# Kernel tuning notes

Measured on AMD Instinct MI355X. Metric: run time of the kernel, lower is better.

The kernel has to match this reference:

```python
import jax, jax.numpy as jnp
import numpy as np

B, S, D = 2, 2048, 1024
H = 16
HD = D // H

def setup_inputs() -> dict:
    key = jax.random.key(0)
    ks = jax.random.split(key, 9)
    s = 1.0 / np.sqrt(D)
    return {
        "x": jax.random.normal(ks[0], (B, S, D), dtype=jnp.float32),
        "Wq": jax.random.normal(ks[1], (D, D), dtype=jnp.float32) * s,
        "bq": jnp.zeros((D,), dtype=jnp.float32),
        "Wk": jax.random.normal(ks[2], (D, D), dtype=jnp.float32) * s,
        "bk": jnp.zeros((D,), dtype=jnp.float32),
        "Wv": jax.random.normal(ks[3], (D, D), dtype=jnp.float32) * s,
        "bv": jnp.zeros((D,), dtype=jnp.float32),
        "Wo": jax.random.normal(ks[4], (D, D), dtype=jnp.float32) * s,
        "bo": jnp.zeros((D,), dtype=jnp.float32),
    }

def reference(x, Wq, bq, Wk, bk, Wv, bv, Wo, bo):
    b, s, d = x.shape
    # torch Linear: y = x @ W.T + b
    def proj(W, bias):
        y = jnp.einsum('bsd,ed->bse', x, W) + bias
        return y.reshape(b, s, H, HD).transpose(0, 2, 1, 3)  # [b,h,s,hd]
    Q = proj(Wq, bq)
    K = proj(Wk, bk)
    V = proj(Wv, bv)
    scale = 1.0 / jnp.sqrt(jnp.float32(HD))
    scores = jnp.einsum('bhqd,bhkd->bhqk', Q, K) * scale  # [b,h,s,s]
    attn = jax.nn.softmax(scores, axis=-1)
    out = jnp.einsum('bhqk,bhkd->bhqd', attn, V)  # [b,h,s,hd]
    out = out.transpose(0, 2, 1, 3).reshape(b, s, d)
    return jnp.einsum('bsd,ed->bse', out, Wo) + bo
```

## Files before the change

kernel.cpp:

```cpp
#include <hip/hip_runtime.h>
#include <stdint.h>


typedef __bf16 bf16x8 __attribute__((ext_vector_type(8)));
typedef float  f32x4  __attribute__((ext_vector_type(4)));
typedef unsigned short u16x8 __attribute__((ext_vector_type(8)));

#define LOG2E 1.44269504088896f
#define FIXED_MAX_BITS 14.4269504088896f

__device__ __forceinline__ unsigned short f2bf(float f) {
    union { float f; unsigned u; } v; v.f = f;
    unsigned r = v.u + 0x7FFFu + ((v.u >> 16) & 1u);
    return (unsigned short)(r >> 16);
}
__device__ __forceinline__ float bf2f(unsigned short u) {
    union { unsigned u; float f; } v; v.u = (unsigned)u << 16; return v.f;
}

__device__ __forceinline__ float exp2_fast(float x) {
#if __has_builtin(__builtin_amdgcn_exp2f)
    return __builtin_amdgcn_exp2f(x);
#else
    return __expf(x * 0.69314718056f);
#endif
}

__device__ __forceinline__ void glds16(const void* g, void* l) {
    __builtin_amdgcn_global_load_lds(
        (__attribute__((address_space(1))) void*)(g),
        (__attribute__((address_space(3))) void*)(l),
        16, 0, 0);
}

__global__ __launch_bounds__(256) void cvt_all(
    const float* __restrict__ x,  const float* __restrict__ Wq,
    const float* __restrict__ Wk, const float* __restrict__ Wv,
    const float* __restrict__ Wo,
    unsigned short* __restrict__ xb,  unsigned short* __restrict__ Wqb,
    unsigned short* __restrict__ Wkb, unsigned short* __restrict__ Wvb,
    unsigned short* __restrict__ Wob)
{
    const int stride = gridDim.x * blockDim.x;
    for (int i = blockIdx.x * blockDim.x + threadIdx.x; i < 2097152; i += stride) {
        const float* src; unsigned short* dst; int j;
        if (i < 1048576) { src = x; dst = xb; j = i; }
        else {
            int t = (i - 1048576) >> 18; j = (i - 1048576) & 262143;
            src = (t == 0) ? Wq : (t == 1) ? Wk : (t == 2) ? Wv : Wo;
            dst = (t == 0) ? Wqb : (t == 1) ? Wkb : (t == 2) ? Wvb : Wob;
        }
        float4 v = ((const float4*)src)[j];
        ushort4 o;
        o.x = f2bf(v.x); o.y = f2bf(v.y); o.z = f2bf(v.z); o.w = f2bf(v.w);
        ((ushort4*)dst)[j] = o;
    }
}

template <int MODE>
__global__ __launch_bounds__(256) void gemm_bt(
    const unsigned short* __restrict__ A,
    const unsigned short* __restrict__ W0,
    const unsigned short* __restrict__ W1,
    const unsigned short* __restrict__ W2,
    const float* __restrict__ b0,
    const float* __restrict__ b1,
    const float* __restrict__ b2,
    unsigned short* __restrict__ outQ,
    unsigned short* __restrict__ outK,
    unsigned short* __restrict__ outV,
    float* __restrict__ outF)
{
    constexpr int BM = (MODE == 0) ? 128 : 64;
    constexpr int FM = BM / 32;
    constexpr int RA = BM / 32;

    __shared__ __attribute__((aligned(16))) unsigned short As[BM * 64];
    __shared__ __attribute__((aligned(16))) unsigned short Bs[128 * 64];

    const int tid  = threadIdx.x;
    const int lane = tid & 63;
    const int wid  = tid >> 6;
    const int quad = lane >> 4;
    const int l16  = lane & 15;

    const int m0 = blockIdx.x * BM;

    const unsigned short* W;
    const float* bias;
    int proj, n0;
    if (MODE == 0) {
        proj = blockIdx.y >> 3;
        n0   = (blockIdx.y & 7) * 128;
        W    = (proj == 0) ? W0 : (proj == 1) ? W1 : W2;
        bias = (proj == 0) ? b0 : (proj == 1) ? b1 : b2;
    } else {
        proj = 0;
        n0   = blockIdx.y * 128;
        W    = W0;
        bias = b0;
    }

    const int wm = (wid >> 1) * (BM / 2);
    const int wn = (wid & 1) * 64;

    f32x4 acc[FM][4];
#pragma unroll
    for (int i = 0; i < FM; ++i)
#pragma unroll
        for (int j = 0; j < 4; ++j)
            acc[i][j] = (f32x4){0.f, 0.f, 0.f, 0.f};

    char* AsB  = (char*)As;
    char* BsB  = (char*)Bs;
    char* ldsA = AsB + wid * 1024;
    char* ldsB = BsB + wid * 1024;

    for (int k0 = 0; k0 < 1024; k0 += 64) {
#pragma unroll
        for (int q = 0; q < RA; ++q) {
            int i   = q * 256 + tid;
            int row = i >> 3;
            int sc  = (i & 7) ^ (row & 7);
            glds16(A + (size_t)(m0 + row) * 1024 + k0 + sc * 8, ldsA + q * 4096);
        }
#pragma unroll
        for (int q = 0; q < 4; ++q) {
            int i   = q * 256 + tid;
            int row = i >> 3;
            int sc  = (i & 7) ^ (row & 7);
            glds16(W + (size_t)(n0 + row) * 1024 + k0 + sc * 8, ldsB + q * 4096);
        }
        __syncthreads();

#pragma unroll
        for (int kh = 0; kh < 2; ++kh) {
            bf16x8 af[FM], bfr[4];
#pragma unroll
            for (int t = 0; t < FM; ++t) {
                int r = wm + t * 16 + l16;
                int c = (kh * 4 + quad) ^ (r & 7);
                af[t] = *(const bf16x8*)(AsB + r * 128 + c * 16);
            }
#pragma unroll
            for (int t = 0; t < 4; ++t) {
                int r = wn + t * 16 + l16;
                int c = (kh * 4 + quad) ^ (r & 7);
                bfr[t] = *(const bf16x8*)(BsB + r * 128 + c * 16);
            }
#pragma unroll
            for (int i = 0; i < FM; ++i)
#pragma unroll
                for (int j = 0; j < 4; ++j)
                    acc[i][j] = __builtin_amdgcn_mfma_f32_16x16x32_bf16(
                        af[i], bfr[j], acc[i][j], 0, 0, 0);
        }
        __syncthreads();
    }

#pragma unroll
    for (int i = 0; i < FM; ++i) {
        const int mrow0 = m0 + wm + i * 16 + quad * 4;
#pragma unroll
        for (int j = 0; j < 4; ++j) {
            const int n  = n0 + wn + j * 16 + l16;
            const float bb = bias[n];
            if (MODE == 1) {
#pragma unroll
                for (int r = 0; r < 4; ++r)
                    outF[(size_t)(mrow0 + r) * 1024 + n] = acc[i][j][r] + bb;
            } else {
                const int h = n >> 6, hd = n & 63;
                if (proj == 2) {
                    const int b = mrow0 >> 11, s = mrow0 & 2047;
                    ushort4 pk;
                    pk.x = f2bf(acc[i][j][0] + bb);
                    pk.y = f2bf(acc[i][j][1] + bb);
                    pk.z = f2bf(acc[i][j][2] + bb);
                    pk.w = f2bf(acc[i][j][3] + bb);
                    *(ushort4*)(outV + ((size_t)((b * 16 + h) * 64 + hd)) * 2048 + s) = pk;
                } else {
                    unsigned short* dst = (proj == 0) ? outQ : outK;
                    const float scl = (proj == 0) ? (0.125f * LOG2E) : 1.0f;
#pragma unroll
                    for (int r = 0; r < 4; ++r) {
                        const int m = mrow0 + r;
                        const int b = m >> 11, s = m & 2047;
                        dst[((size_t)((b * 16 + h) * 2048 + s)) * 64 + hd] =
                            f2bf((acc[i][j][r] + bb) * scl);
                    }
                }
            }
        }
    }
}

__global__ __launch_bounds__(256, 4) void attn_kernel(
    const unsigned short* __restrict__ Qb,
    const unsigned short* __restrict__ Kb,
    const unsigned short* __restrict__ Vtb,
    unsigned short* __restrict__ OP,
    float* __restrict__ LS)
{
    __shared__ __attribute__((aligned(16))) unsigned short Ks[128 * 64];
    __shared__ __attribute__((aligned(16))) unsigned short Vs[2 * 64 * 64];

    const int tid  = threadIdx.x;
    const int lane = tid & 63;
    const int wid  = tid >> 6;
    const int quad = lane >> 4;
    const int l16  = lane & 15;
    const int l7   = l16 & 7;

    const int half = blockIdx.x & 1;
    const int q0   = (blockIdx.x >> 1) * 128 + wid * 32;
    const int hb   = blockIdx.y;
    const int bq   = hb >> 4, hh = hb & 15;

    const unsigned short* Qh  = Qb  + (size_t)hb * 2048 * 64;
    const unsigned short* Kh  = Kb  + (size_t)hb * 2048 * 64;
    const unsigned short* Vth = Vtb + (size_t)hb * 64 * 2048;

    bf16x8 qf[2][2];
#pragma unroll
    for (int qt = 0; qt < 2; ++qt) {
        const unsigned short* qp = Qh + (size_t)(q0 + qt * 16 + l16) * 64 + quad * 8;
        qf[qt][0] = *(const bf16x8*)(qp);
        qf[qt][1] = *(const bf16x8*)(qp + 32);
    }

    f32x4 o[4][2];
#pragma unroll
    for (int ht = 0; ht < 4; ++ht)
#pragma unroll
        for (int qt = 0; qt < 2; ++qt)
            o[ht][qt] = (f32x4){0.f, 0.f, 0.f, 0.f};
    float lsum[2] = {0.f, 0.f};

    char* KsB  = (char*)Ks;
    char* ldsK = KsB + wid * 1024;

    const int base_row = 8 * (l16 >> 2) + (l16 & 3);
    const int kp0 = ((quad) ^ l7) * 16;
    const int kp1 = ((4 + quad) ^ l7) * 16;
    const int vrow = l16 * 128;

    const int kc0 = half * 1024;
    for (int kc = kc0; kc < kc0 + 1024; kc += 128) {
#pragma unroll
        for (int q = 0; q < 4; ++q) {
            int i   = q * 256 + tid;
            int row = i >> 3;
            int g   = (row & 3) | (((row >> 3) & 1) << 2);
            int ch  = (i & 7) ^ g;
            glds16(Kh + (size_t)(kc + row) * 64 + ch * 8, ldsK + q * 4096);
        }
#pragma unroll
        for (int sub = 0; sub < 2; ++sub)
#pragma unroll
            for (int q = 0; q < 2; ++q) {
                int i   = q * 256 + tid;
                int row = i >> 3;
                int ch  = (i & 7) ^ (row & 7);
                glds16(Vth + (size_t)row * 2048 + kc + sub * 64 + ch * 8,
                       (char*)Vs + sub * 8192 + wid * 1024 + q * 4096);
            }
        __syncthreads();

#pragma unroll
        for (int st32 = 0; st32 < 4; ++st32) {
            const char* krb = KsB + (st32 * 32 + base_row) * 128;
            bf16x8 kf00 = *(const bf16x8*)(krb + kp0);
            bf16x8 kf01 = *(const bf16x8*)(krb + kp1);
            bf16x8 kf10 = *(const bf16x8*)(krb + 512 + kp0);
            bf16x8 kf11 = *(const bf16x8*)(krb + 512 + kp1);

            const f32x4 mi = (f32x4){-FIXED_MAX_BITS, -FIXED_MAX_BITS,
                                     -FIXED_MAX_BITS, -FIXED_MAX_BITS};
            f32x4 s00 = mi, s01 = mi, s10 = mi, s11 = mi;
            s00 = __builtin_amdgcn_mfma_f32_16x16x32_bf16(kf00, qf[0][0], s00, 0, 0, 0);
            s00 = __builtin_amdgcn_mfma_f32_16x16x32_bf16(kf01, qf[0][1], s00, 0, 0, 0);
            s01 = __builtin_amdgcn_mfma_f32_16x16x32_bf16(kf10, qf[0][0], s01, 0, 0, 0);
            s01 = __builtin_amdgcn_mfma_f32_16x16x32_bf16(kf11, qf[0][1], s01, 0, 0, 0);
            s10 = __builtin_amdgcn_mfma_f32_16x16x32_bf16(kf00, qf[1][0], s10, 0, 0, 0);
            s10 = __builtin_amdgcn_mfma_f32_16x16x32_bf16(kf01, qf[1][1], s10, 0, 0, 0);
            s11 = __builtin_amdgcn_mfma_f32_16x16x32_bf16(kf10, qf[1][0], s11, 0, 0, 0);
            s11 = __builtin_amdgcn_mfma_f32_16x16x32_bf16(kf11, qf[1][1], s11, 0, 0, 0);

            bf16x8 p8[2];
#pragma unroll
            for (int qt = 0; qt < 2; ++qt) {
                const f32x4 sA = qt ? s10 : s00;
                const f32x4 sB = qt ? s11 : s01;
                float e0 = exp2_fast(sA[0]), e1 = exp2_fast(sA[1]);
                float e2 = exp2_fast(sA[2]), e3 = exp2_fast(sA[3]);
                float e4 = exp2_fast(sB[0]), e5 = exp2_fast(sB[1]);
                float e6 = exp2_fast(sB[2]), e7 = exp2_fast(sB[3]);
                lsum[qt] += ((e0 + e1) + (e2 + e3)) + ((e4 + e5) + (e6 + e7));
                u16x8 up;
                up[0] = f2bf(e0); up[1] = f2bf(e1); up[2] = f2bf(e2); up[3] = f2bf(e3);
                up[4] = f2bf(e4); up[5] = f2bf(e5); up[6] = f2bf(e6); up[7] = f2bf(e7);
                p8[qt] = __builtin_bit_cast(bf16x8, up);
            }

            const int voff = (st32 >> 1) * 8192 + vrow
                           + ((((st32 & 1) * 4 + quad) ^ l7) * 16);
#pragma unroll
            for (int ht = 0; ht < 4; ++ht) {
                const bf16x8 vf = *(const bf16x8*)((char*)Vs + voff + ht * 2048);
                o[ht][0] = __builtin_amdgcn_mfma_f32_16x16x32_bf16(vf, p8[0], o[ht][0], 0, 0, 0);
                o[ht][1] = __builtin_amdgcn_mfma_f32_16x16x32_bf16(vf, p8[1], o[ht][1], 0, 0, 0);
            }
        }
        __syncthreads();
    }

    float lt[2];
#pragma unroll
    for (int qt = 0; qt < 2; ++qt) {
        float s = lsum[qt];
        s += __shfl_xor(s, 16);
        s += __shfl_xor(s, 32);
        lt[qt] = s;
    }

    unsigned short* OPh = OP + (size_t)half * 4096 * 1024;
#pragma unroll
    for (int qt = 0; qt < 2; ++qt) {
        const size_t row = (size_t)(bq * 2048 + q0 + qt * 16 + l16);
#pragma unroll
        for (int ht = 0; ht < 4; ++ht) {
            ushort4 pk;
            pk.x = f2bf(o[ht][qt][0]);
            pk.y = f2bf(o[ht][qt][1]);
            pk.z = f2bf(o[ht][qt][2]);
            pk.w = f2bf(o[ht][qt][3]);
            *(ushort4*)(OPh + row * 1024 + hh * 64 + ht * 16 + quad * 4) = pk;
        }
    }
    if (quad == 0) {
        LS[half * 65536 + hb * 2048 + q0 + l16]      = lt[0];
        LS[half * 65536 + hb * 2048 + q0 + 16 + l16] = lt[1];
    }
}

__global__ __launch_bounds__(256) void attn_reduce(
    const unsigned short* __restrict__ OP,
    const float* __restrict__ LS,
    unsigned short* __restrict__ attnb)
{
    const size_t idx = ((size_t)blockIdx.x * 256 + threadIdx.x) * 8;
    const int row = (int)(idx >> 10);
    const int col = (int)(idx & 1023);
    const int bh  = ((row >> 11) << 4) + (col >> 6);
    const int q   = row & 2047;
    const float l = LS[bh * 2048 + q] + LS[65536 + bh * 2048 + q];
    const float rl = 1.0f / l;

    ushort4 a0 = *(const ushort4*)(OP + idx);
    ushort4 a1 = *(const ushort4*)(OP + idx + 4);
    ushort4 b0 = *(const ushort4*)(OP + 4194304 + idx);
    ushort4 b1 = *(const ushort4*)(OP + 4194304 + idx + 4);
    ushort4 o0, o1;
    o0.x = f2bf((bf2f(a0.x) + bf2f(b0.x)) * rl);
    o0.y = f2bf((bf2f(a0.y) + bf2f(b0.y)) * rl);
    o0.z = f2bf((bf2f(a0.z) + bf2f(b0.z)) * rl);
    o0.w = f2bf((bf2f(a0.w) + bf2f(b0.w)) * rl);
    o1.x = f2bf((bf2f(a1.x) + bf2f(b1.x)) * rl);
    o1.y = f2bf((bf2f(a1.y) + bf2f(b1.y)) * rl);
    o1.z = f2bf((bf2f(a1.z) + bf2f(b1.z)) * rl);
    o1.w = f2bf((bf2f(a1.w) + bf2f(b1.w)) * rl);
    *(ushort4*)(attnb + idx)     = o0;
    *(ushort4*)(attnb + idx + 4) = o1;
}

extern "C" void kernel_launch(void* const* d_in, const int* in_sizes, int n_in,
                              void* d_out, int out_size, void* d_ws, size_t ws_size,
                              hipStream_t stream) {
    (void)in_sizes; (void)n_in; (void)out_size; (void)ws_size;

    const float* x  = (const float*)d_in[0];
    const float* Wq = (const float*)d_in[1];
    const float* bq = (const float*)d_in[2];
    const float* Wk = (const float*)d_in[3];
    const float* bk = (const float*)d_in[4];
    const float* Wv = (const float*)d_in[5];
    const float* bv = (const float*)d_in[6];
    const float* Wo = (const float*)d_in[7];
    const float* bo = (const float*)d_in[8];

    char* ws = (char*)d_ws;
    const size_t MB = 1024 * 1024;
    unsigned short* xb    = (unsigned short*)(ws + 0);
    unsigned short* Wqb   = (unsigned short*)(ws + 8  * MB);
    unsigned short* Wkb   = (unsigned short*)(ws + 10 * MB);
    unsigned short* Wvb   = (unsigned short*)(ws + 12 * MB);
    unsigned short* Wob   = (unsigned short*)(ws + 14 * MB);
    unsigned short* Qb    = (unsigned short*)(ws + 16 * MB);
    unsigned short* Kb    = (unsigned short*)(ws + 24 * MB);
    unsigned short* Vtb   = (unsigned short*)(ws + 32 * MB);
    unsigned short* attnb = (unsigned short*)(ws + 40 * MB);
    unsigned short* OP    = (unsigned short*)(ws + 48 * MB);
    float*          LSb   = (float*)(ws + 64 * MB);

    cvt_all<<<dim3(1024), dim3(256), 0, stream>>>(
        x, Wq, Wk, Wv, Wo, xb, Wqb, Wkb, Wvb, Wob);

    gemm_bt<0><<<dim3(32, 24), dim3(256), 0, stream>>>(
        xb, Wqb, Wkb, Wvb, bq, bk, bv, Qb, Kb, Vtb, nullptr);

    attn_kernel<<<dim3(32, 32), dim3(256), 0, stream>>>(Qb, Kb, Vtb, OP, LSb);

    attn_reduce<<<dim3(2048), dim3(256), 0, stream>>>(OP, LSb, attnb);

    gemm_bt<1><<<dim3(64, 8), dim3(256), 0, stream>>>(
        attnb, Wob, nullptr, nullptr, bo, nullptr, nullptr,
        nullptr, nullptr, nullptr, (float*)d_out);
}
```

Baseline: 198.6 us.

## Double-buffer GEMM LDS, remap attention block order, use native bf16 conversion

The projection GEMM now double-buffers its A and B tiles in LDS. It issues the next k-tile's global-to-LDS loads before computing on the current one, so memory latency can overlap the MFMA work. The attention kernel remaps its block index so that eight consecutive blocks cover different heads in an interleaved order, which changes L2 locality and the spread across CUs. The manual round-to-nearest float-to-bf16 conversion of softmax probabilities is replaced by native __bf16 casts, which may map to hardware conversion instructions. Doubling LDS per block may reduce GEMM occupancy, and the loop appears to issue the next stage without a barrier between compute and the overwrite of the alternate buffer.

Measured after the change: 190.5 us. 4.1% less time.

```diff
diff --git a/kernel.cpp b/kernel.cpp
--- a/kernel.cpp
+++ b/kernel.cpp
@@ -4,7 +4,6 @@
 
 typedef __bf16 bf16x8 __attribute__((ext_vector_type(8)));
 typedef float  f32x4  __attribute__((ext_vector_type(4)));
-typedef unsigned short u16x8 __attribute__((ext_vector_type(8)));
 
 #define LOG2E 1.44269504088896f
 #define FIXED_MAX_BITS 14.4269504088896f
@@ -75,8 +74,8 @@
     constexpr int FM = BM / 32;
     constexpr int RA = BM / 32;
 
-    __shared__ __attribute__((aligned(16))) unsigned short As[BM * 64];
-    __shared__ __attribute__((aligned(16))) unsigned short Bs[128 * 64];
+    __shared__ __attribute__((aligned(16))) unsigned short As[2 * BM * 64];
+    __shared__ __attribute__((aligned(16))) unsigned short Bs[2 * 128 * 64];
 
     const int tid  = threadIdx.x;
     const int lane = tid & 63;
@@ -111,12 +110,12 @@
         for (int j = 0; j < 4; ++j)
             acc[i][j] = (f32x4){0.f, 0.f, 0.f, 0.f};
 
-    char* AsB  = (char*)As;
-    char* BsB  = (char*)Bs;
-    char* ldsA = AsB + wid * 1024;
-    char* ldsB = BsB + wid * 1024;
-
-    for (int k0 = 0; k0 < 1024; k0 += 64) {
+    char* AsB = (char*)As;
+    char* BsB = (char*)Bs;
+
+    auto stageAB = [&](int k0, int buf) {
+        char* ldsA = AsB + buf * (BM * 128) + wid * 1024;
+        char* ldsB = BsB + buf * 16384 + wid * 1024;
 #pragma unroll
         for (int q = 0; q < RA; ++q) {
             int i   = q * 256 + tid;
@@ -131,7 +130,17 @@
             int sc  = (i & 7) ^ (row & 7);
             glds16(W + (size_t)(n0 + row) * 1024 + k0 + sc * 8, ldsB + q * 4096);
         }
-        __syncthreads();
+    };
+
+    stageAB(0, 0);
+    __syncthreads();
+
+    for (int k0 = 0; k0 < 1024; k0 += 64) {
+        const int cur = (k0 >> 6) & 1;
+        if (k0 + 64 < 1024) stageAB(k0 + 64, cur ^ 1);
+
+        const char* AsC = AsB + cur * (BM * 128);
+        const char* BsC = BsB + cur * 16384;
 
 #pragma unroll
         for (int kh = 0; kh < 2; ++kh) {
@@ -140,13 +149,13 @@
             for (int t = 0; t < FM; ++t) {
                 int r = wm + t * 16 + l16;
                 int c = (kh * 4 + quad) ^ (r & 7);
-                af[t] = *(const bf16x8*)(AsB + r * 128 + c * 16);
+                af[t] = *(const bf16x8*)(AsC + r * 128 + c * 16);
             }
 #pragma unroll
             for (int t = 0; t < 4; ++t) {
                 int r = wn + t * 16 + l16;
                 int c = (kh * 4 + quad) ^ (r & 7);
-                bfr[t] = *(const bf16x8*)(BsB + r * 128 + c * 16);
+                bfr[t] = *(const bf16x8*)(BsC + r * 128 + c * 16);
             }
 #pragma unroll
             for (int i = 0; i < FM; ++i)
@@ -212,9 +221,14 @@
     const int l16  = lane & 15;
     const int l7   = l16 & 7;
 
-    const int half = blockIdx.x & 1;
-    const int q0   = (blockIdx.x >> 1) * 128 + wid * 32;
-    const int hb   = blockIdx.y;
+    const int bid  = blockIdx.x + (blockIdx.y << 5);
+    const int c8   = bid & 7;
+    const int t    = bid >> 3;
+    const int hb   = c8 + ((t >> 5) << 3);
+    const int u    = t & 31;
+    const int qt16 = u >> 1;
+    const int half = u & 1;
+    const int q0   = qt16 * 128 + wid * 32;
     const int bq   = hb >> 4, hh = hb & 15;
 
     const unsigned short* Qh  = Qb  + (size_t)hb * 2048 * 64;
@@ -297,10 +311,12 @@
                 float e4 = exp2_fast(sB[0]), e5 = exp2_fast(sB[1]);
                 float e6 = exp2_fast(sB[2]), e7 = exp2_fast(sB[3]);
                 lsum[qt] += ((e0 + e1) + (e2 + e3)) + ((e4 + e5) + (e6 + e7));
-                u16x8 up;
-                up[0] = f2bf(e0); up[1] = f2bf(e1); up[2] = f2bf(e2); up[3] = f2bf(e3);
-                up[4] = f2bf(e4); up[5] = f2bf(e5); up[6] = f2bf(e6); up[7] = f2bf(e7);
-                p8[qt] = __builtin_bit_cast(bf16x8, up);
+                bf16x8 p;
+                p[0] = (__bf16)e0; p[1] = (__bf16)e1;
+                p[2] = (__bf16)e2; p[3] = (__bf16)e3;
+                p[4] = (__bf16)e4; p[5] = (__bf16)e5;
+                p[6] = (__bf16)e6; p[7] = (__bf16)e7;
+                p8[qt] = p;
             }
 
             const int voff = (st32 >> 1) * 8192 + vrow
```
